# Optimization experiments

Hardware: AMD Instinct MI355X
Metric: run time of the kernel (lower is better)

## Reference

```python
import jax, jax.numpy as jnp
import numpy as np

B, S, D = 4, 2048, 1024
H, DK, DV = 16, 64, 64
NEG = -1e10


def setup_inputs() -> dict:
    key = jax.random.key(0)
    ks = jax.random.split(key, 7)
    queries = jax.random.normal(ks[0], (B, S, D), dtype=jnp.float32)
    keys = jax.random.normal(ks[1], (B, S, D), dtype=jnp.float32)
    values = jax.random.normal(ks[2], (B, S, D), dtype=jnp.float32)
    mask = jnp.ones((B, S, S), dtype=jnp.int32)
    # per-head Linear weights, torch layout [out, in]; stacked over heads
    Wq = jax.random.normal(ks[3], (H, DK, D), dtype=jnp.float32) / np.sqrt(D)
    Wk = jax.random.normal(ks[4], (H, DK, D), dtype=jnp.float32) / np.sqrt(D)
    Wv = jax.random.normal(ks[5], (H, DV, D), dtype=jnp.float32) / np.sqrt(D)
    Wo = jax.random.normal(ks[6], (D, H * DV), dtype=jnp.float32) / np.sqrt(H * DV)
    return {"queries": queries, "keys": keys, "values": values, "mask": mask,
            "Wq": Wq, "Wk": Wk, "Wv": Wv, "Wo": Wo}


def reference(queries, keys, values, mask, Wq, Wk, Wv, Wo):
    # per-head projections, vectorized over heads: y = x @ W_h^T
    q = jnp.einsum('bsd,hkd->bhsk', queries, Wq)   # [B,H,S,DK]
    k = jnp.einsum('btd,hkd->bhtk', keys, Wk)      # [B,H,S,DK]
    v = jnp.einsum('btd,hvd->bhtv', values, Wv)    # [B,H,S,DV]
    scores = jnp.einsum('bhsk,bhtk->bhst', q, k) / jnp.sqrt(jnp.asarray(DK, q.dtype))
    scores = jnp.where(mask[:, None, :, :] == 0, jnp.asarray(NEG, q.dtype), scores)
    attn = jax.nn.softmax(scores, axis=-1)
    out = jnp.einsum('bhst,bhtv->bhsv', attn, v)   # [B,H,S,DV]
    # torch.cat over heads on last dim == head-major concat per position
    out = out.transpose(0, 2, 1, 3).reshape(B, S, H * DV)
    return out @ Wo.T
```

## Files before the change

### kernel.cpp

```cpp
#include <hip/hip_runtime.h>
#include <stdint.h>

typedef __attribute__((ext_vector_type(4))) float f32x4;
typedef __attribute__((ext_vector_type(8))) __bf16 bf16x8;
typedef __attribute__((ext_vector_type(4))) __bf16 bf16x4;
typedef __attribute__((ext_vector_type(4))) short s16x4;
typedef __attribute__((ext_vector_type(2))) uint32_t u32x2;

#define MFMA16(a, b, c) __builtin_amdgcn_mfma_f32_16x16x32_bf16(a, b, c, 0, 0, 0)
#define MFMA16K16(a, b, c) __builtin_amdgcn_mfma_f32_16x16x16bf16_1k(a, b, c, 0, 0, 0)

#define B_ 4
#define S_ 2048
#define D_ 1024
#define H_ 16
#define NEG_ -1e10f
#define QSCALE 0.180336880f

__device__ __forceinline__ float ex2(float x) { return __builtin_amdgcn_exp2f(x); }

__device__ __forceinline__ void glds16(const void* gsrc, void* ldst) {
  __builtin_amdgcn_global_load_lds(
      (__attribute__((address_space(1))) void*)(gsrc),
      (__attribute__((address_space(3))) void*)(ldst),
      16, 0, 0);
}

__device__ __forceinline__ uint32_t pack_bf16(float a, float b) {
  uint32_t ua = (uint32_t)__builtin_bit_cast(unsigned short, (__bf16)a);
  uint32_t ub = (uint32_t)__builtin_bit_cast(unsigned short, (__bf16)b);
  return ua | (ub << 16);
}

__global__ __launch_bounds__(256) void prep(
    const float* __restrict__ xq, const float* __restrict__ xk, const float* __restrict__ xv,
    const float* __restrict__ wq, const float* __restrict__ wk, const float* __restrict__ wv,
    const float* __restrict__ wo,
    __bf16* __restrict__ oxq, __bf16* __restrict__ oxk, __bf16* __restrict__ oxv,
    __bf16* __restrict__ owq, __bf16* __restrict__ owk, __bf16* __restrict__ owv,
    __bf16* __restrict__ owo,
    const int* __restrict__ mask, uint32_t* __restrict__ bits, int* __restrict__ flags) {
  int bid = blockIdx.x, tid = threadIdx.x;
  __shared__ int andred;
  if (bid < 24576) {
    int z = bid >> 13, xb = bid & 8191;
    const float* in = (z == 0) ? xq : (z == 1) ? xk : xv;
    __bf16* out = (z == 0) ? oxq : (z == 1) ? oxk : oxv;
    int i = (xb * 256 + tid) * 4;
    float4 v = *(const float4*)(in + i);
    bf16x4 o;
    o.x = (__bf16)v.x; o.y = (__bf16)v.y; o.z = (__bf16)v.z; o.w = (__bf16)v.w;
    *(bf16x4*)(out + i) = o;
  } else if (bid < 28672) {
    int m = bid - 24576;
    int z = m >> 10, wb = m & 1023;
    const float* in = (z == 0) ? wq : (z == 1) ? wk : (z == 2) ? wv : wo;
    __bf16* out = (z == 0) ? owq : (z == 1) ? owk : (z == 2) ? owv : owo;
    int i = (wb * 256 + tid) * 4;
    float4 v = *(const float4*)(in + i);
    bf16x4 o;
    o.x = (__bf16)v.x; o.y = (__bf16)v.y; o.z = (__bf16)v.z; o.w = (__bf16)v.w;
    *(bf16x4*)(out + i) = o;
  } else {
    int m = bid - 28672;
    int tt = m & 15, st = (m >> 4) & 15, b = m >> 8;
    int w = tid >> 6, lane = tid & 63;
    if (tid == 0) andred = 1;
    __syncthreads();
    unsigned long long all1 = ~0ull;
    for (int rr = 0; rr < 32; rr++) {
      int srow = st * 128 + w * 32 + rr;
      #pragma unroll
      for (int half = 0; half < 2; half++) {
        int c = tt * 128 + half * 64 + lane;
        int mm = mask[((size_t)b * S_ + srow) * S_ + c];
        unsigned long long bal = __ballot(mm != 0);
        all1 &= bal;
        if (lane == 0) {
          uint32_t* dst = &bits[((size_t)b * S_ + srow) * 64 + tt * 4 + half * 2];
          dst[0] = (uint32_t)bal;
          dst[1] = (uint32_t)(bal >> 32);
        }
      }
    }
    if (all1 != ~0ull) atomicAnd(&andred, 0);
    __syncthreads();
    if (tid == 0) flags[(b * 16 + st) * 16 + tt] = andred;
  }
}

template <int MODE>
__global__ __launch_bounds__(256, 3) void gemm_bt(
    const __bf16* __restrict__ A0, const __bf16* __restrict__ A1, const __bf16* __restrict__ A2,
    const __bf16* __restrict__ W0, const __bf16* __restrict__ W1, const __bf16* __restrict__ W2,
    void* O0, void* O1, void* O2) {
  const int K = 1024;
  const __bf16* PA; const __bf16* PB; void* O;
  int pa_t, pb_t;
  if (MODE == 0) {
    if (blockIdx.z == 0)      { PA = W0; PB = A0; O = O0; pa_t = blockIdx.x; pb_t = blockIdx.y; }
    else if (blockIdx.z == 1) { PA = W1; PB = A1; O = O1; pa_t = blockIdx.x; pb_t = blockIdx.y; }
    else                      { PA = A2; PB = W2; O = O2; pa_t = blockIdx.y; pb_t = blockIdx.x; }
  } else { PA = W0; PB = A0; O = O0; pa_t = blockIdx.x; pb_t = blockIdx.y; }

  __shared__ __align__(16) __bf16 As[128 * 64];
  __shared__ __align__(16) __bf16 Bs[128 * 64];
  int tid = threadIdx.x, lane = tid & 63, w = tid >> 6;
  int wm = w >> 1, wn = w & 1;
  int g = lane >> 4, l15 = lane & 15;
  f32x4 acc[4][4] = {};
  const __bf16* Ablk = PA + (size_t)(pa_t * 128) * K;
  const __bf16* Bblk = PB + (size_t)(pb_t * 128) * K;

  for (int kt = 0; kt < K; kt += 64) {
    __syncthreads();
    #pragma unroll
    for (int r = 0; r < 4; r++) {
      int C = r * 256 + tid;
      int row = C >> 3, c = C & 7;
      int c0 = c ^ (row & 7);
      glds16(Ablk + (size_t)row * K + kt + c0 * 8, (char*)As + C * 16);
      glds16(Bblk + (size_t)row * K + kt + c0 * 8, (char*)Bs + C * 16);
    }
    __syncthreads();
    #pragma unroll
    for (int kkq = 0; kkq < 2; kkq++) {
      bf16x8 af[4], bfr[4];
      #pragma unroll
      for (int i = 0; i < 4; i++) {
        int row = wm * 64 + i * 16 + l15;
        int ch = (kkq * 4 + g) ^ (row & 7);
        af[i] = *(const bf16x8*)((const char*)As + row * 128 + ch * 16);
      }
      #pragma unroll
      for (int j = 0; j < 4; j++) {
        int row = wn * 64 + j * 16 + l15;
        int ch = (kkq * 4 + g) ^ (row & 7);
        bfr[j] = *(const bf16x8*)((const char*)Bs + row * 128 + ch * 16);
      }
      #pragma unroll
      for (int i = 0; i < 4; i++)
        #pragma unroll
        for (int j = 0; j < 4; j++)
          acc[i][j] = MFMA16(af[i], bfr[j], acc[i][j]);
    }
  }

  if (MODE == 1) {
    #pragma unroll
    for (int i = 0; i < 4; i++)
      #pragma unroll
      for (int j = 0; j < 4; j++) {
        int n0 = pa_t * 128 + wm * 64 + i * 16 + g * 4;
        int m = pb_t * 128 + wn * 64 + j * 16 + l15;
        *(f32x4*)((float*)O + (size_t)m * 1024 + n0) = acc[i][j];
      }
  } else if (blockIdx.z == 2) {
    #pragma unroll
    for (int i = 0; i < 4; i++)
      #pragma unroll
      for (int j = 0; j < 4; j++) {
        int s0 = pa_t * 128 + wm * 64 + i * 16 + g * 4;
        int dvg = pb_t * 128 + wn * 64 + j * 16 + l15;
        int b = s0 >> 11, s = s0 & 2047;
        int h = dvg >> 6, dv = dvg & 63;
        bf16x4 o;
        #pragma unroll
        for (int r = 0; r < 4; r++) o[r] = (__bf16)acc[i][j][r];
        *(bf16x4*)((__bf16*)O + (((size_t)b * 16 + h) * 64 + dv) * 2048 + s) = o;
      }
  } else {
    float scale = (blockIdx.z == 0) ? QSCALE : 1.0f;
    #pragma unroll
    for (int i = 0; i < 4; i++)
      #pragma unroll
      for (int j = 0; j < 4; j++) {
        int dkg = pa_t * 128 + wm * 64 + i * 16 + g * 4;
        int sg = pb_t * 128 + wn * 64 + j * 16 + l15;
        int h = dkg >> 6, dk = dkg & 63;
        int b = sg >> 11, s = sg & 2047;
        bf16x4 o;
        #pragma unroll
        for (int r = 0; r < 4; r++) o[r] = (__bf16)(acc[i][j][r] * scale);
        *(bf16x4*)((__bf16*)O + (((size_t)b * 16 + h) * 2048 + s) * 64 + dk) = o;
      }
  }
}

__global__ __launch_bounds__(256, 2) void attn(
    const __bf16* __restrict__ qp, const __bf16* __restrict__ kp,
    const __bf16* __restrict__ vt_, __bf16* __restrict__ aout,
    const uint32_t* __restrict__ bits, const int* __restrict__ flags) {
  int qt = blockIdx.x, bh = blockIdx.y, b = bh >> 4, h = bh & 15;
  int tid = threadIdx.x, lane = tid & 63, w = tid >> 6;
  int g = lane >> 4, l15 = lane & 15;

  __shared__ __align__(16) char smem[32768];
  char* Klds = smem;
  char* Vlds = smem + 16384;

  const __bf16* Qg = qp + ((size_t)bh * S_ + qt * 128) * 64;
  const __bf16* Kg = kp + (size_t)bh * S_ * 64;
  const __bf16* Vg = vt_ + (size_t)bh * 64 * S_;

  #pragma unroll
  for (int r = 0; r < 4; r++) {
    int C = r * 256 + tid;
    int row = C >> 3, c = C & 7, c0 = c ^ (row & 7);
    glds16(Qg + row * 64 + c0 * 8, Klds + C * 16);
  }
  __syncthreads();
  bf16x8 qf[2][2];
  #pragma unroll
  for (int i = 0; i < 2; i++)
    #pragma unroll
    for (int kkq = 0; kkq < 2; kkq++) {
      int row = w * 32 + i * 16 + l15;
      int ch = (kkq * 4 + g) ^ (row & 7);
      qf[i][kkq] = *(const bf16x8*)(Klds + row * 128 + ch * 16);
    }
  __syncthreads();

  f32x4 oacc[4][2] = {};
  float mst[2] = {-INFINITY, -INFINITY}, lst[2] = {0.f, 0.f};

  for (int kt = 0; kt < 16; kt++) {
    const __bf16* Ks = Kg + (size_t)kt * 128 * 64;
    #pragma unroll
    for (int r = 0; r < 4; r++) {
      int C = r * 256 + tid;
      int row = C >> 3, c = C & 7, c0 = c ^ (row & 7);
      glds16(Ks + row * 64 + c0 * 8, Klds + C * 16);
    }
    #pragma unroll
    for (int r = 0; r < 4; r++) {
      int C = r * 256 + tid;
      int row = C >> 4, c = C & 15;
      int c0 = (c & 8) | ((c & 7) ^ (row & 7));
      glds16(Vg + (size_t)row * S_ + kt * 128 + c0 * 8, Vlds + C * 16);
    }
    __syncthreads();

    f32x4 sacc[2][8] = {};
    #pragma unroll
    for (int jt = 0; jt < 8; jt++) {
      int row = jt * 16 + l15;
      bf16x8 kf0 = *(const bf16x8*)(Klds + row * 128 + (g ^ (row & 7)) * 16);
      bf16x8 kf1 = *(const bf16x8*)(Klds + row * 128 + ((4 + g) ^ (row & 7)) * 16);
      sacc[0][jt] = MFMA16(kf0, qf[0][0], sacc[0][jt]);
      sacc[0][jt] = MFMA16(kf1, qf[0][1], sacc[0][jt]);
      sacc[1][jt] = MFMA16(kf0, qf[1][0], sacc[1][jt]);
      sacc[1][jt] = MFMA16(kf1, qf[1][1], sacc[1][jt]);
    }

    if (!flags[(b * 16 + qt) * 16 + kt]) {
      #pragma unroll
      for (int i = 0; i < 2; i++) {
        int srow = qt * 128 + w * 32 + i * 16 + l15;
        const uint32_t* bw = &bits[((size_t)b * S_ + srow) * 64 + kt * 4];
        uint32_t mw[4] = {bw[0], bw[1], bw[2], bw[3]};
        #pragma unroll
        for (int jt = 0; jt < 8; jt++)
          #pragma unroll
          for (int r = 0; r < 4; r++) {
            int bitpos = (jt & 1) * 16 + g * 4 + r;
            if (!((mw[jt >> 1] >> bitpos) & 1)) sacc[i][jt][r] = NEG_;
          }
      }
    }

    float alpha[2];
    #pragma unroll
    for (int i = 0; i < 2; i++) {
      float mx = -INFINITY;
      #pragma unroll
      for (int jt = 0; jt < 8; jt++)
        #pragma unroll
        for (int r = 0; r < 4; r++) mx = fmaxf(mx, sacc[i][jt][r]);
      mx = fmaxf(mx, __shfl_xor(mx, 16));
      mx = fmaxf(mx, __shfl_xor(mx, 32));
      float mnew = fmaxf(mst[i], mx);
      alpha[i] = ex2(mst[i] - mnew);
      mst[i] = mnew;
    }
    #pragma unroll
    for (int vt = 0; vt < 4; vt++)
      #pragma unroll
      for (int i = 0; i < 2; i++)
        #pragma unroll
        for (int r = 0; r < 4; r++) oacc[vt][i][r] *= alpha[i];

    float sum[2] = {0.f, 0.f};
    #pragma unroll
    for (int jt = 0; jt < 8; jt++) {
      s16x4 pf[2];
      #pragma unroll
      for (int i = 0; i < 2; i++) {
        float p0 = ex2(sacc[i][jt][0] - mst[i]);
        float p1 = ex2(sacc[i][jt][1] - mst[i]);
        float p2 = ex2(sacc[i][jt][2] - mst[i]);
        float p3 = ex2(sacc[i][jt][3] - mst[i]);
        sum[i] += (p0 + p1) + (p2 + p3);
        u32x2 t;
        t.x = pack_bf16(p0, p1);
        t.y = pack_bf16(p2, p3);
        pf[i] = __builtin_bit_cast(s16x4, t);
      }
      int ch = jt * 2 + (g >> 1);
      #pragma unroll
      for (int vt = 0; vt < 4; vt++) {
        int row = vt * 16 + l15;
        int chs = (ch & 8) | ((ch & 7) ^ (row & 7));
        s16x4 vv = *(const s16x4*)(Vlds + row * 256 + chs * 16 + (g & 1) * 8);
        oacc[vt][0] = MFMA16K16(vv, pf[0], oacc[vt][0]);
        oacc[vt][1] = MFMA16K16(vv, pf[1], oacc[vt][1]);
      }
    }
    #pragma unroll
    for (int i = 0; i < 2; i++) {
      sum[i] += __shfl_xor(sum[i], 16);
      sum[i] += __shfl_xor(sum[i], 32);
      lst[i] = lst[i] * alpha[i] + sum[i];
    }
    __syncthreads();
  }

  #pragma unroll
  for (int i = 0; i < 2; i++) {
    float inv = 1.0f / lst[i];
    int srow = qt * 128 + w * 32 + i * 16 + l15;
    #pragma unroll
    for (int vt = 0; vt < 4; vt++) {
      bf16x4 o;
      #pragma unroll
      for (int r = 0; r < 4; r++) o[r] = (__bf16)(oacc[vt][i][r] * inv);
      *(bf16x4*)(aout + ((size_t)b * S_ + srow) * 1024 + h * 64 + vt * 16 + g * 4) = o;
    }
  }
}

extern "C" void kernel_launch(void* const* d_in, const int* in_sizes, int n_in,
                              void* d_out, int out_size, void* d_ws, size_t ws_size,
                              hipStream_t stream) {
  const float* queries = (const float*)d_in[0];
  const float* keys    = (const float*)d_in[1];
  const float* values  = (const float*)d_in[2];
  const int*   mask    = (const int*)d_in[3];
  const float* Wq      = (const float*)d_in[4];
  const float* Wk      = (const float*)d_in[5];
  const float* Wv      = (const float*)d_in[6];
  const float* Wo      = (const float*)d_in[7];

  char* ws = (char*)d_ws;
  __bf16* Xq  = (__bf16*)(ws + 0);
  __bf16* Xk  = (__bf16*)(ws + 16777216);
  __bf16* Xv  = (__bf16*)(ws + 33554432);
  __bf16* Wqb = (__bf16*)(ws + 50331648);
  __bf16* Wkb = (__bf16*)(ws + 52428800);
  __bf16* Wvb = (__bf16*)(ws + 54525952);
  __bf16* Wob = (__bf16*)(ws + 56623104);
  __bf16* qp  = (__bf16*)(ws + 58720256);
  __bf16* kp  = (__bf16*)(ws + 75497472);
  __bf16* vT  = (__bf16*)(ws + 92274688);
  uint32_t* bits = (uint32_t*)(ws + 109051904);
  int* flags     = (int*)(ws + 111149056);
  __bf16* aout = Xq;

  prep<<<29696, 256, 0, stream>>>(queries, keys, values, Wq, Wk, Wv, Wo,
                                  Xq, Xk, Xv, Wqb, Wkb, Wvb, Wob,
                                  mask, bits, flags);

  gemm_bt<0><<<dim3(8, 64, 3), 256, 0, stream>>>(Xq, Xk, Xv, Wqb, Wkb, Wvb,
                                                 (void*)qp, (void*)kp, (void*)vT);

  attn<<<dim3(16, 64), 256, 0, stream>>>(qp, kp, vT, aout, bits, flags);

  gemm_bt<1><<<dim3(8, 64, 1), 256, 0, stream>>>(aout, nullptr, nullptr, Wob, nullptr, nullptr,
                                                 (void*)d_out, nullptr, nullptr);
}
```

Before: 430.0 us.

## Chunk attention inner loop with lazy rescale and MFMA row sums

Splits each 128-key tile into four 32-key chunks so score accumulators shrink, and raises the occupancy target to 3 blocks per CU. The running max is only updated when a new max exceeds the old one by more than 8 (log2 units), which skips most rescales of the output accumulators. Row sums are computed with an extra MFMA against a ones vector instead of shuffles and adds, and MFMA sections get raised wave priority. The trade-offs are more MFMA work, tighter register pressure, and a risk of spills under the higher occupancy bound.

```diff
diff --git a/kernel.cpp b/kernel.cpp
--- a/kernel.cpp
+++ b/kernel.cpp
@@ -187,7 +187,7 @@
   }
 }
 
-__global__ __launch_bounds__(256, 2) void attn(
+__global__ __launch_bounds__(256, 3) void attn(
     const __bf16* __restrict__ qp, const __bf16* __restrict__ kp,
     const __bf16* __restrict__ vt_, __bf16* __restrict__ aout,
     const uint32_t* __restrict__ bits, const int* __restrict__ flags) {
@@ -222,7 +222,10 @@
   __syncthreads();
 
   f32x4 oacc[4][2] = {};
-  float mst[2] = {-INFINITY, -INFINITY}, lst[2] = {0.f, 0.f};
+  f32x4 sumacc[2] = {};
+  float mst[2] = {-INFINITY, -INFINITY};
+  const f32x4 zero4 = {0.f, 0.f, 0.f, 0.f};
+  const s16x4 ones = {(short)0x3F80, (short)0x3F80, (short)0x3F80, (short)0x3F80};
 
   for (int kt = 0; kt < 16; kt++) {
     const __bf16* Ks = Kg + (size_t)kt * 128 * 64;
@@ -241,93 +244,107 @@
     }
     __syncthreads();
 
-    f32x4 sacc[2][8] = {};
-    #pragma unroll
-    for (int jt = 0; jt < 8; jt++) {
-      int row = jt * 16 + l15;
-      bf16x8 kf0 = *(const bf16x8*)(Klds + row * 128 + (g ^ (row & 7)) * 16);
-      bf16x8 kf1 = *(const bf16x8*)(Klds + row * 128 + ((4 + g) ^ (row & 7)) * 16);
-      sacc[0][jt] = MFMA16(kf0, qf[0][0], sacc[0][jt]);
-      sacc[0][jt] = MFMA16(kf1, qf[0][1], sacc[0][jt]);
-      sacc[1][jt] = MFMA16(kf0, qf[1][0], sacc[1][jt]);
-      sacc[1][jt] = MFMA16(kf1, qf[1][1], sacc[1][jt]);
-    }
-
-    if (!flags[(b * 16 + qt) * 16 + kt]) {
+    int fl = flags[(b * 16 + qt) * 16 + kt];
+
+    #pragma unroll
+    for (int cch = 0; cch < 4; cch++) {
+      f32x4 sc[2][2];
+      __builtin_amdgcn_s_setprio(1);
+      #pragma unroll
+      for (int jj = 0; jj < 2; jj++) {
+        int row = (cch * 2 + jj) * 16 + l15;
+        bf16x8 kf0 = *(const bf16x8*)(Klds + row * 128 + (g ^ (row & 7)) * 16);
+        bf16x8 kf1 = *(const bf16x8*)(Klds + row * 128 + ((4 + g) ^ (row & 7)) * 16);
+        sc[0][jj] = MFMA16(kf0, qf[0][0], zero4);
+        sc[0][jj] = MFMA16(kf1, qf[0][1], sc[0][jj]);
+        sc[1][jj] = MFMA16(kf0, qf[1][0], zero4);
+        sc[1][jj] = MFMA16(kf1, qf[1][1], sc[1][jj]);
+      }
+      __builtin_amdgcn_s_setprio(0);
+
+      if (!fl) {
+        #pragma unroll
+        for (int i = 0; i < 2; i++) {
+          int srow = qt * 128 + w * 32 + i * 16 + l15;
+          uint32_t mw = bits[((size_t)b * S_ + srow) * 64 + kt * 4 + cch];
+          #pragma unroll
+          for (int jj = 0; jj < 2; jj++)
+            #pragma unroll
+            for (int r = 0; r < 4; r++)
+              if (!((mw >> (jj * 16 + g * 4 + r)) & 1)) sc[i][jj][r] = NEG_;
+        }
+      }
+
+      float mx[2];
       #pragma unroll
       for (int i = 0; i < 2; i++) {
-        int srow = qt * 128 + w * 32 + i * 16 + l15;
-        const uint32_t* bw = &bits[((size_t)b * S_ + srow) * 64 + kt * 4];
-        uint32_t mw[4] = {bw[0], bw[1], bw[2], bw[3]};
-        #pragma unroll
-        for (int jt = 0; jt < 8; jt++)
+        float a = fmaxf(fmaxf(sc[i][0][0], sc[i][0][1]), fmaxf(sc[i][0][2], sc[i][0][3]));
+        float bb = fmaxf(fmaxf(sc[i][1][0], sc[i][1][1]), fmaxf(sc[i][1][2], sc[i][1][3]));
+        float m = fmaxf(a, bb);
+        m = fmaxf(m, __shfl_xor(m, 16));
+        m = fmaxf(m, __shfl_xor(m, 32));
+        mx[i] = m;
+      }
+
+      bool need = (mx[0] > mst[0] + 8.f) || (mx[1] > mst[1] + 8.f);
+      if (__any(need)) {
+        float alpha[2];
+        #pragma unroll
+        for (int i = 0; i < 2; i++) {
+          float mnew = fmaxf(mst[i], mx[i]);
+          alpha[i] = ex2(mst[i] - mnew);
+          mst[i] = mnew;
+        }
+        #pragma unroll
+        for (int vt = 0; vt < 4; vt++)
           #pragma unroll
-          for (int r = 0; r < 4; r++) {
-            int bitpos = (jt & 1) * 16 + g * 4 + r;
-            if (!((mw[jt >> 1] >> bitpos) & 1)) sacc[i][jt][r] = NEG_;
-          }
-      }
-    }
-
-    float alpha[2];
-    #pragma unroll
-    for (int i = 0; i < 2; i++) {
-      float mx = -INFINITY;
-      #pragma unroll
-      for (int jt = 0; jt < 8; jt++)
-        #pragma unroll
-        for (int r = 0; r < 4; r++) mx = fmaxf(mx, sacc[i][jt][r]);
-      mx = fmaxf(mx, __shfl_xor(mx, 16));
-      mx = fmaxf(mx, __shfl_xor(mx, 32));
-      float mnew = fmaxf(mst[i], mx);
-      alpha[i] = ex2(mst[i] - mnew);
-      mst[i] = mnew;
-    }
-    #pragma unroll
-    for (int vt = 0; vt < 4; vt++)
-      #pragma unroll
-      for (int i = 0; i < 2; i++)
-        #pragma unroll
-        for (int r = 0; r < 4; r++) oacc[vt][i][r] *= alpha[i];
-
-    float sum[2] = {0.f, 0.f};
-    #pragma unroll
-    for (int jt = 0; jt < 8; jt++) {
-      s16x4 pf[2];
-      #pragma unroll
-      for (int i = 0; i < 2; i++) {
-        float p0 = ex2(sacc[i][jt][0] - mst[i]);
-        float p1 = ex2(sacc[i][jt][1] - mst[i]);
-        float p2 = ex2(sacc[i][jt][2] - mst[i]);
-        float p3 = ex2(sacc[i][jt][3] - mst[i]);
-        sum[i] += (p0 + p1) + (p2 + p3);
-        u32x2 t;
-        t.x = pack_bf16(p0, p1);
-        t.y = pack_bf16(p2, p3);
-        pf[i] = __builtin_bit_cast(s16x4, t);
-      }
-      int ch = jt * 2 + (g >> 1);
-      #pragma unroll
-      for (int vt = 0; vt < 4; vt++) {
-        int row = vt * 16 + l15;
-        int chs = (ch & 8) | ((ch & 7) ^ (row & 7));
-        s16x4 vv = *(const s16x4*)(Vlds + row * 256 + chs * 16 + (g & 1) * 8);
-        oacc[vt][0] = MFMA16K16(vv, pf[0], oacc[vt][0]);
-        oacc[vt][1] = MFMA16K16(vv, pf[1], oacc[vt][1]);
-      }
-    }
-    #pragma unroll
-    for (int i = 0; i < 2; i++) {
-      sum[i] += __shfl_xor(sum[i], 16);
-      sum[i] += __shfl_xor(sum[i], 32);
-      lst[i] = lst[i] * alpha[i] + sum[i];
+          for (int i = 0; i < 2; i++)
+            #pragma unroll
+            for (int r = 0; r < 4; r++) oacc[vt][i][r] *= alpha[i];
+        #pragma unroll
+        for (int i = 0; i < 2; i++)
+          #pragma unroll
+          for (int r = 0; r < 4; r++) sumacc[i][r] *= alpha[i];
+      }
+
+      s16x4 pf[2][2];
+      #pragma unroll
+      for (int jj = 0; jj < 2; jj++)
+        #pragma unroll
+        for (int i = 0; i < 2; i++) {
+          float p0 = ex2(sc[i][jj][0] - mst[i]);
+          float p1 = ex2(sc[i][jj][1] - mst[i]);
+          float p2 = ex2(sc[i][jj][2] - mst[i]);
+          float p3 = ex2(sc[i][jj][3] - mst[i]);
+          u32x2 t;
+          t.x = pack_bf16(p0, p1);
+          t.y = pack_bf16(p2, p3);
+          pf[jj][i] = __builtin_bit_cast(s16x4, t);
+        }
+
+      __builtin_amdgcn_s_setprio(1);
+      #pragma unroll
+      for (int jj = 0; jj < 2; jj++) {
+        int ch = (cch * 2 + jj) * 2 + (g >> 1);
+        #pragma unroll
+        for (int vt = 0; vt < 4; vt++) {
+          int row = vt * 16 + l15;
+          int chs = (ch & 8) | ((ch & 7) ^ (row & 7));
+          s16x4 vv = *(const s16x4*)(Vlds + row * 256 + chs * 16 + (g & 1) * 8);
+          oacc[vt][0] = MFMA16K16(vv, pf[jj][0], oacc[vt][0]);
+          oacc[vt][1] = MFMA16K16(vv, pf[jj][1], oacc[vt][1]);
+        }
+        sumacc[0] = MFMA16K16(ones, pf[jj][0], sumacc[0]);
+        sumacc[1] = MFMA16K16(ones, pf[jj][1], sumacc[1]);
+      }
+      __builtin_amdgcn_s_setprio(0);
     }
     __syncthreads();
   }
 
   #pragma unroll
   for (int i = 0; i < 2; i++) {
-    float inv = 1.0f / lst[i];
+    float inv = 1.0f / sumacc[i][0];
     int srow = qt * 128 + w * 32 + i * 16 + l15;
     #pragma unroll
     for (int vt = 0; vt < 4; vt++) {
```

After: 440.0 us. +2.3%, slower.

## Double-buffer K/V tiles in attention and compute row sums via MFMA

Applied to the files above, without the earlier changes.

The attention kernel now keeps two K/V LDS buffers (64KB) and prefetches the next tile while computing on the current one, replacing the load-then-sync pattern with a single vmcnt wait and barrier per iteration. Softmax row sums are accumulated with an extra MFMA against a ones vector instead of scalar adds and shuffles. Rescaling of the output accumulator is skipped unless the running max grows by more than a threshold (lazy rescale). MFMA sections also get priority bumps. The larger LDS footprint may reduce occupancy to fewer blocks per CU, and the lazy rescale adds some numerical risk.

```diff
diff --git a/kernel.cpp b/kernel.cpp
--- a/kernel.cpp
+++ b/kernel.cpp
@@ -195,9 +195,7 @@
   int tid = threadIdx.x, lane = tid & 63, w = tid >> 6;
   int g = lane >> 4, l15 = lane & 15;
 
-  __shared__ __align__(16) char smem[32768];
-  char* Klds = smem;
-  char* Vlds = smem + 16384;
+  __shared__ __align__(16) char smem[65536];
 
   const __bf16* Qg = qp + ((size_t)bh * S_ + qt * 128) * 64;
   const __bf16* Kg = kp + (size_t)bh * S_ * 64;
@@ -207,7 +205,7 @@
   for (int r = 0; r < 4; r++) {
     int C = r * 256 + tid;
     int row = C >> 3, c = C & 7, c0 = c ^ (row & 7);
-    glds16(Qg + row * 64 + c0 * 8, Klds + C * 16);
+    glds16(Qg + row * 64 + c0 * 8, smem + C * 16);
   }
   __syncthreads();
   bf16x8 qf[2][2];
@@ -217,43 +215,64 @@
     for (int kkq = 0; kkq < 2; kkq++) {
       int row = w * 32 + i * 16 + l15;
       int ch = (kkq * 4 + g) ^ (row & 7);
-      qf[i][kkq] = *(const bf16x8*)(Klds + row * 128 + ch * 16);
+      qf[i][kkq] = *(const bf16x8*)(smem + row * 128 + ch * 16);
     }
   __syncthreads();
 
-  f32x4 oacc[4][2] = {};
-  float mst[2] = {-INFINITY, -INFINITY}, lst[2] = {0.f, 0.f};
-
-  for (int kt = 0; kt < 16; kt++) {
-    const __bf16* Ks = Kg + (size_t)kt * 128 * 64;
+  auto stageKV = [&](int kt2, int p) {
+    char* Kl = smem + p * 32768;
+    char* Vl = Kl + 16384;
+    const __bf16* Ks = Kg + (size_t)kt2 * 128 * 64;
     #pragma unroll
     for (int r = 0; r < 4; r++) {
       int C = r * 256 + tid;
       int row = C >> 3, c = C & 7, c0 = c ^ (row & 7);
-      glds16(Ks + row * 64 + c0 * 8, Klds + C * 16);
+      glds16(Ks + row * 64 + c0 * 8, Kl + C * 16);
     }
     #pragma unroll
     for (int r = 0; r < 4; r++) {
       int C = r * 256 + tid;
       int row = C >> 4, c = C & 15;
       int c0 = (c & 8) | ((c & 7) ^ (row & 7));
-      glds16(Vg + (size_t)row * S_ + kt * 128 + c0 * 8, Vlds + C * 16);
-    }
-    __syncthreads();
-
-    f32x4 sacc[2][8] = {};
+      glds16(Vg + (size_t)row * S_ + kt2 * 128 + c0 * 8, Vl + C * 16);
+    }
+  };
+
+  f32x4 oacc[4][2] = {};
+  f32x4 sumacc[2] = {};
+  float mst[2] = {-INFINITY, -INFINITY};
+  const f32x4 zero4 = {0.f, 0.f, 0.f, 0.f};
+  const s16x4 ones = {(short)0x3F80, (short)0x3F80, (short)0x3F80, (short)0x3F80};
+
+  stageKV(0, 0);
+  asm volatile("s_waitcnt vmcnt(0)" ::: "memory");
+  __builtin_amdgcn_s_barrier();
+  __builtin_amdgcn_sched_barrier(0);
+
+  for (int kt = 0; kt < 16; kt++) {
+    int cur = kt & 1;
+    if (kt + 1 < 16) stageKV(kt + 1, cur ^ 1);
+    __builtin_amdgcn_sched_barrier(0);
+
+    const char* Klds = smem + cur * 32768;
+    const char* Vlds = Klds + 16384;
+    int fl = flags[(b * 16 + qt) * 16 + kt];
+
+    f32x4 sacc[2][8];
+    __builtin_amdgcn_s_setprio(1);
     #pragma unroll
     for (int jt = 0; jt < 8; jt++) {
       int row = jt * 16 + l15;
       bf16x8 kf0 = *(const bf16x8*)(Klds + row * 128 + (g ^ (row & 7)) * 16);
       bf16x8 kf1 = *(const bf16x8*)(Klds + row * 128 + ((4 + g) ^ (row & 7)) * 16);
-      sacc[0][jt] = MFMA16(kf0, qf[0][0], sacc[0][jt]);
+      sacc[0][jt] = MFMA16(kf0, qf[0][0], zero4);
       sacc[0][jt] = MFMA16(kf1, qf[0][1], sacc[0][jt]);
-      sacc[1][jt] = MFMA16(kf0, qf[1][0], sacc[1][jt]);
+      sacc[1][jt] = MFMA16(kf0, qf[1][0], zero4);
       sacc[1][jt] = MFMA16(kf1, qf[1][1], sacc[1][jt]);
     }
-
-    if (!flags[(b * 16 + qt) * 16 + kt]) {
+    __builtin_amdgcn_s_setprio(0);
+
+    if (!fl) {
       #pragma unroll
       for (int i = 0; i < 2; i++) {
         int srow = qt * 128 + w * 32 + i * 16 + l15;
@@ -269,28 +288,42 @@
       }
     }
 
-    float alpha[2];
+    float mx[2];
     #pragma unroll
     for (int i = 0; i < 2; i++) {
-      float mx = -INFINITY;
-      #pragma unroll
-      for (int jt = 0; jt < 8; jt++)
-        #pragma unroll
-        for (int r = 0; r < 4; r++) mx = fmaxf(mx, sacc[i][jt][r]);
-      mx = fmaxf(mx, __shfl_xor(mx, 16));
-      mx = fmaxf(mx, __shfl_xor(mx, 32));
-      float mnew = fmaxf(mst[i], mx);
-      alpha[i] = ex2(mst[i] - mnew);
-      mst[i] = mnew;
-    }
-    #pragma unroll
-    for (int vt = 0; vt < 4; vt++)
+      float m = -INFINITY;
+      #pragma unroll
+      for (int jt = 0; jt < 8; jt++) {
+        float a = fmaxf(fmaxf(sacc[i][jt][0], sacc[i][jt][1]),
+                        fmaxf(sacc[i][jt][2], sacc[i][jt][3]));
+        m = fmaxf(m, a);
+      }
+      m = fmaxf(m, __shfl_xor(m, 16));
+      m = fmaxf(m, __shfl_xor(m, 32));
+      mx[i] = m;
+    }
+
+    bool need = (mx[0] > mst[0] + 8.f) || (mx[1] > mst[1] + 8.f);
+    if (__any(need)) {
+      float alpha[2];
+      #pragma unroll
+      for (int i = 0; i < 2; i++) {
+        float mnew = fmaxf(mst[i], mx[i]);
+        alpha[i] = ex2(mst[i] - mnew);
+        mst[i] = mnew;
+      }
+      #pragma unroll
+      for (int vt = 0; vt < 4; vt++)
+        #pragma unroll
+        for (int i = 0; i < 2; i++)
+          #pragma unroll
+          for (int r = 0; r < 4; r++) oacc[vt][i][r] *= alpha[i];
       #pragma unroll
       for (int i = 0; i < 2; i++)
         #pragma unroll
-        for (int r = 0; r < 4; r++) oacc[vt][i][r] *= alpha[i];
-
-    float sum[2] = {0.f, 0.f};
+        for (int r = 0; r < 4; r++) sumacc[i][r] *= alpha[i];
+    }
+
     #pragma unroll
     for (int jt = 0; jt < 8; jt++) {
       s16x4 pf[2];
@@ -300,13 +333,13 @@
         float p1 = ex2(sacc[i][jt][1] - mst[i]);
         float p2 = ex2(sacc[i][jt][2] - mst[i]);
         float p3 = ex2(sacc[i][jt][3] - mst[i]);
-        sum[i] += (p0 + p1) + (p2 + p3);
         u32x2 t;
         t.x = pack_bf16(p0, p1);
         t.y = pack_bf16(p2, p3);
         pf[i] = __builtin_bit_cast(s16x4, t);
       }
       int ch = jt * 2 + (g >> 1);
+      __builtin_amdgcn_s_setprio(1);
       #pragma unroll
       for (int vt = 0; vt < 4; vt++) {
         int row = vt * 16 + l15;
@@ -315,19 +348,19 @@
         oacc[vt][0] = MFMA16K16(vv, pf[0], oacc[vt][0]);
         oacc[vt][1] = MFMA16K16(vv, pf[1], oacc[vt][1]);
       }
-    }
-    #pragma unroll
-    for (int i = 0; i < 2; i++) {
-      sum[i] += __shfl_xor(sum[i], 16);
-      sum[i] += __shfl_xor(sum[i], 32);
-      lst[i] = lst[i] * alpha[i] + sum[i];
-    }
-    __syncthreads();
+      sumacc[0] = MFMA16K16(ones, pf[0], sumacc[0]);
+      sumacc[1] = MFMA16K16(ones, pf[1], sumacc[1]);
+      __builtin_amdgcn_s_setprio(0);
+    }
+
+    asm volatile("s_waitcnt vmcnt(0)" ::: "memory");
+    __builtin_amdgcn_s_barrier();
+    __builtin_amdgcn_sched_barrier(0);
   }
 
   #pragma unroll
   for (int i = 0; i < 2; i++) {
-    float inv = 1.0f / lst[i];
+    float inv = 1.0f / sumacc[i][0];
     int srow = qt * 128 + w * 32 + i * 16 + l15;
     #pragma unroll
     for (int vt = 0; vt < 4; vt++) {
```

New measurement: 424.9 us. Within noise of the previous version (-1.2%).
